# Optimization experiments

Measured on AMD Instinct MI355X. Metric: run time of the kernel, lower is better.

## Reference

```python
import jax, jax.numpy as jnp
import numpy as np

N_NODES = 100000
N_EDGES = 1600000
FEAT = 32
HID = 32
N_GRAPHS = 64


def setup_inputs() -> dict:
    key = jax.random.key(0)
    ks = jax.random.split(key, 12)
    x = jax.random.normal(ks[0], (N_NODES, FEAT), dtype=jnp.float32)
    edge_index = jax.random.randint(ks[1], (2, N_EDGES), 0, N_NODES, dtype=jnp.int64)
    batch = jnp.sort(jax.random.randint(ks[2], (N_NODES,), 0, N_GRAPHS, dtype=jnp.int64))
    # ChebConv (K=3) params: one linear per Chebyshev order + shared bias
    W_cheb = jax.random.normal(ks[3], (3, FEAT, HID), dtype=jnp.float32) * 0.1
    b_cheb = jnp.zeros((HID,), dtype=jnp.float32)
    # MLP head 32 -> 1024 -> 512 -> 4
    W1 = jax.random.normal(ks[4], (HID, 1024), dtype=jnp.float32) * 0.05
    b1 = jnp.zeros((1024,), dtype=jnp.float32)
    W2 = jax.random.normal(ks[5], (1024, 512), dtype=jnp.float32) * 0.05
    b2 = jnp.zeros((512,), dtype=jnp.float32)
    W3 = jax.random.normal(ks[6], (512, 4), dtype=jnp.float32) * 0.05
    b3 = jnp.zeros((4,), dtype=jnp.float32)
    return {"x": x, "edge_index": edge_index, "batch": batch,
            "W_cheb": W_cheb, "b_cheb": b_cheb,
            "W1": W1, "b1": b1, "W2": W2, "b2": b2, "W3": W3, "b3": b3}


def reference(x, edge_index, batch, W_cheb, b_cheb, W1, b1, W2, b2, W3, b3):
    row, col = edge_index[0], edge_index[1]  # source, target
    n = x.shape[0]
    # symmetric normalization of scaled Laplacian (lambda_max=2, no self loops):
    # L_hat = -D^{-1/2} A D^{-1/2}
    deg = jax.ops.segment_sum(jnp.ones((row.shape[0],), x.dtype), row, num_segments=n)
    dis = jnp.where(deg > 0, jax.lax.rsqrt(jnp.where(deg > 0, deg, 1.0)), 0.0)
    norm = -(dis[row] * dis[col])  # [E]

    def prop(h):  # L_hat @ h via gather -> scale -> scatter-add
        return jax.ops.segment_sum(norm[:, None] * h[row], col, num_segments=n)

    # Chebyshev recursion: T0=x, T1=L_hat x, T2=2 L_hat T1 - T0
    Tx0 = x
    Tx1 = prop(Tx0)
    Tx2 = 2.0 * prop(Tx1) - Tx0
    h = Tx0 @ W_cheb[0] + Tx1 @ W_cheb[1] + Tx2 @ W_cheb[2] + b_cheb  # [N, HID]
    # global max pool per graph
    g = jax.ops.segment_max(h, batch, num_segments=N_GRAPHS)  # [B, HID]
    # MLP head (dropout/LeakyReLU defined but unused in original forward)
    h1 = jax.nn.relu(g @ W1 + b1)
    h2 = jax.nn.relu(h1 @ W2 + b2)
    return h2 @ W3 + b3  # [B, 4]
```

## Files before the change

### kernel.cpp

```cpp
#include <hip/hip_runtime.h>
#include <hip/hip_fp16.h>


#define NT 256
#define NTS 1024
#define BSHIFT 8
#define BSIZE 256
#define HB 256
#define CAPC 48
#define CAPR 64
#define CAP 5120

typedef _Float16 half8 __attribute__((ext_vector_type(8)));
typedef float f32x4 __attribute__((ext_vector_type(4)));

__device__ __forceinline__ void atomicMaxFloat(float* addr, float val) {
    if (val >= 0.0f) atomicMax((int*)addr, __float_as_int(val));
    else             atomicMin((unsigned int*)addr, __float_as_uint(val));
}

#define ACC8(raw)                                        \
    do {                                                 \
        const __half2* hp_ = (const __half2*)&(raw);     \
        float2 f0_ = __half22float2(hp_[0]);             \
        float2 f1_ = __half22float2(hp_[1]);             \
        float2 f2_ = __half22float2(hp_[2]);             \
        float2 f3_ = __half22float2(hp_[3]);             \
        a0 += f0_.x; a1 += f0_.y; a2 += f1_.x; a3 += f1_.y; \
        a4 += f2_.x; a5 += f2_.y; a6 += f3_.x; a7 += f3_.y; \
    } while (0)

__global__ __launch_bounds__(512) void k_init(float* __restrict__ g,
                                              const float* __restrict__ Wc,
                                              _Float16* __restrict__ wfrag,
                                              int* __restrict__ bcur,
                                              int* __restrict__ rcur, int NBK) {
    int tid = threadIdx.x;
    for (int i = tid; i < 64 * 32; i += 512) g[i] = -__builtin_inff();
    if (tid < 384) {
        int combo = tid >> 6, lane = tid & 63;
        int mat = combo >> 1, n = combo & 1;
        int m = lane & 15, quad = lane >> 4;
        #pragma unroll
        for (int j = 0; j < 8; j++)
            wfrag[(size_t)combo * 512 + lane * 8 + j] =
                (_Float16)Wc[mat * 1024 + (quad * 8 + j) * 32 + n * 16 + m];
    }
    if (tid < NBK) {
        bcur[tid] = tid * CAP;
        rcur[tid] = tid * CAP;
    }
}

__global__ __launch_bounds__(NTS) void k_bscatter(const int* __restrict__ row,
                                                  const int* __restrict__ col,
                                                  int* __restrict__ bcur,
                                                  int* __restrict__ rcur,
                                                  int* __restrict__ ebuck,
                                                  unsigned char* __restrict__ rbuck,
                                                  int E, int NBK, int epb) {
    __shared__ int cntc[512], cntr[512];
    __shared__ int basec[512], baser[512];
    __shared__ int cstage[512 * CAPC];
    __shared__ unsigned char rstage[512 * CAPR];
    int tid = threadIdx.x;
    if (tid < 512) { cntc[tid] = 0; cntr[tid] = 0; }
    __syncthreads();
    int start = blockIdx.x * epb;
    int end = min(start + epb, E);
    for (int e = start + tid; e < end; e += NTS) {
        int r = row[e], c = col[e];
        int bc_ = c >> BSHIFT;
        int li = atomicAdd(&cntc[bc_], 1);
        if (li < CAPC)
            cstage[bc_ * CAPC + li] = (r << BSHIFT) | (c & (BSIZE - 1));
        int br_ = r >> BSHIFT;
        int lj = atomicAdd(&cntr[br_], 1);
        if (lj < CAPR)
            rstage[br_ * CAPR + lj] = (unsigned char)(r & (BSIZE - 1));
    }
    __syncthreads();
    if (tid < 512) {
        int n = min(cntc[tid], CAPC);
        basec[tid] = n ? atomicAdd(&bcur[tid], n) : 0;
    } else {
        int b = tid - 512;
        int n = min(cntr[b], CAPR);
        baser[b] = n ? atomicAdd(&rcur[b], n) : 0;
    }
    __syncthreads();
    int warp = tid >> 6, lane = tid & 63;
    for (int b = warp; b < NBK; b += (NTS >> 6)) {
        int n = min(cntc[b], CAPC);
        int base = basec[b];
        for (int i = lane; i < n; i += 64)
            ebuck[base + i] = cstage[b * CAPC + i];
    }
    for (int b = warp; b < NBK; b += (NTS >> 6)) {
        int n = min(cntr[b], CAPR);
        int base = baser[b];
        for (int i = lane; i < n; i += 64)
            rbuck[base + i] = rstage[b * CAPR + i];
    }
}

__global__ __launch_bounds__(NT) void k_prep(
    const int* __restrict__ rcur, const unsigned char* __restrict__ rbuck,
    const int* __restrict__ bcur, const int* __restrict__ ebuck,
    const float* __restrict__ x,
    float* __restrict__ dis, float* __restrict__ rdis,
    __half* __restrict__ xh, __half* __restrict__ xsh,
    int* __restrict__ offs, int* __restrict__ entries, int N) {
    __shared__ int cnt[1024];
    __shared__ int tsum[256];
    __shared__ float sdis[256];
    int b = blockIdx.x, tid = threadIdx.x;
    int rbase = b * CAP, rend = rcur[b];
    int ebase = b * CAP, eend = bcur[b];
    cnt[tid] = 0; cnt[tid + 256] = 0; cnt[tid + 512] = 0; cnt[tid + 768] = 0;
    __syncthreads();
    for (int e = rbase + tid; e < rend; e += NT)
        atomicAdd(&cnt[rbuck[e]], 1);
    __syncthreads();
    int dcount = cnt[tid];
    int node = (b << BSHIFT) + tid;
    float d = (dcount > 0) ? rsqrtf((float)dcount) : 0.0f;
    if (node < N) {
        dis[node] = d;
        rdis[node] = (dcount > 0) ? sqrtf((float)dcount) : 0.0f;
    }
    sdis[tid] = d;
    __syncthreads();
    cnt[tid] = 0; cnt[tid + 256] = 0; cnt[tid + 512] = 0; cnt[tid + 768] = 0;
    __syncthreads();
    for (int e = ebase + tid; e < eend; e += NT) {
        int pv = ebuck[e];
        atomicAdd(&cnt[((pv & (BSIZE - 1)) << 2) | ((pv >> BSHIFT) >> 15)], 1);
    }
    __syncthreads();
    int s0 = cnt[tid * 4], s1 = cnt[tid * 4 + 1], s2 = cnt[tid * 4 + 2], s3 = cnt[tid * 4 + 3];
    int tot = s0 + s1 + s2 + s3;
    tsum[tid] = tot;
    __syncthreads();
    for (int off = 1; off < 256; off <<= 1) {
        int t = (tid >= off) ? tsum[tid - off] : 0;
        __syncthreads();
        tsum[tid] += t;
        __syncthreads();
    }
    int excl = tsum[tid] - tot;
    if (node < N) offs[node] = ((ebase + excl) << 9) | tot;
    cnt[tid * 4]     = ebase + excl;
    cnt[tid * 4 + 1] = ebase + excl + s0;
    cnt[tid * 4 + 2] = ebase + excl + s0 + s1;
    cnt[tid * 4 + 3] = ebase + excl + s0 + s1 + s2;
    __syncthreads();
    for (int e = ebase + tid; e < eend; e += NT) {
        int pv = ebuck[e];
        int src = pv >> BSHIFT;
        int li = atomicAdd(&cnt[((pv & (BSIZE - 1)) << 2) | (src >> 15)], 1);
        entries[li] = src;
    }
    int nodebase = b << BSHIFT;
    for (int i4 = tid; i4 < 2048; i4 += NT) {
        int gnode = nodebase + (i4 >> 3);
        if (gnode >= N) break;
        float4 v = ((const float4*)x)[(size_t)nodebase * 8 + i4];
        float dd = sdis[i4 >> 3];
        float2 o, os;
        ((__half2*)&o)[0] = __floats2half2_rn(v.x, v.y);
        ((__half2*)&o)[1] = __floats2half2_rn(v.z, v.w);
        ((__half2*)&os)[0] = __floats2half2_rn(dd * v.x, dd * v.y);
        ((__half2*)&os)[1] = __floats2half2_rn(dd * v.z, dd * v.w);
        ((float2*)xh)[(size_t)nodebase * 8 + i4] = o;
        ((float2*)xsh)[(size_t)nodebase * 8 + i4] = os;
    }
}

__global__ __launch_bounds__(NT) void k_prop1(const int* __restrict__ offs,
                                              const int* __restrict__ entries,
                                              const float* __restrict__ dis,
                                              const __half* __restrict__ xsh,
                                              __half* __restrict__ xs2h, int N) {
    int idx = blockIdx.x * blockDim.x + threadIdx.x;
    int node = idx >> 3, sp = (idx >> 2) & 1, q = idx & 3;
    if (node >= N) return;
    int pv = offs[node];
    int s = pv >> 9, deg = pv & 511;
    int mid = s + (deg >> 1), t = s + deg;
    int lo = sp ? mid : s;
    int hi = sp ? t : mid;
    float a0 = 0, a1 = 0, a2 = 0, a3 = 0, a4 = 0, a5 = 0, a6 = 0, a7 = 0;
    int e = lo;
    for (; e + 4 <= hi; e += 4) {
        int r0 = entries[e], r1 = entries[e + 1], r2 = entries[e + 2], r3 = entries[e + 3];
        float4 w0 = *(const float4*)(xsh + (size_t)r0 * 32 + q * 8);
        float4 w1 = *(const float4*)(xsh + (size_t)r1 * 32 + q * 8);
        float4 w2 = *(const float4*)(xsh + (size_t)r2 * 32 + q * 8);
        float4 w3 = *(const float4*)(xsh + (size_t)r3 * 32 + q * 8);
        ACC8(w0); ACC8(w1); ACC8(w2); ACC8(w3);
    }
    for (; e < hi; e++) {
        int r = entries[e];
        float4 w = *(const float4*)(xsh + (size_t)r * 32 + q * 8);
        ACC8(w);
    }
    a0 += __shfl_xor(a0, 4); a1 += __shfl_xor(a1, 4);
    a2 += __shfl_xor(a2, 4); a3 += __shfl_xor(a3, 4);
    a4 += __shfl_xor(a4, 4); a5 += __shfl_xor(a5, 4);
    a6 += __shfl_xor(a6, 4); a7 += __shfl_xor(a7, 4);
    if (sp == 0) {
        float d = dis[node];
        float sd = -d * d;
        float4 ov;
        ((__half2*)&ov)[0] = __floats2half2_rn(sd * a0, sd * a1);
        ((__half2*)&ov)[1] = __floats2half2_rn(sd * a2, sd * a3);
        ((__half2*)&ov)[2] = __floats2half2_rn(sd * a4, sd * a5);
        ((__half2*)&ov)[3] = __floats2half2_rn(sd * a6, sd * a7);
        *(float4*)(xs2h + (size_t)node * 32 + q * 8) = ov;
    }
}

__global__ __launch_bounds__(NT) void k_combine_f(
    const int* __restrict__ offs, const int* __restrict__ entries,
    const float* __restrict__ dis, const float* __restrict__ rdis,
    const __half* __restrict__ xs2h, const _Float16* __restrict__ xh,
    const _Float16* __restrict__ wfrag, const float* __restrict__ bc,
    const int* __restrict__ batch, float* __restrict__ g, int N) {
    __shared__ float sb[32];
    __shared__ float sp2[64][33];
    __shared__ float hs[64][33];
    __shared__ float lmax[64][32];
    __shared__ int sbatch[64];
    __shared__ int s_blo, s_bhi;

    int tid = threadIdx.x;
    if (tid < 32) sb[tid] = bc[tid];
    int rowbase = blockIdx.x * 64;
    if (tid >= 64 && tid < 128) {
        int gr = rowbase + tid - 64;
        sbatch[tid - 64] = (gr < N) ? batch[gr] : -1;
    }

    int node_l = tid >> 2, q = tid & 3;
    int gnode = rowbase + node_l;
    if (gnode < N) {
        int pv = offs[gnode];
        int s = pv >> 9, t = s + (pv & 511);
        float a0 = 0, a1 = 0, a2 = 0, a3 = 0, a4 = 0, a5 = 0, a6 = 0, a7 = 0;
        int e = s;
        for (; e + 4 <= t; e += 4) {
            int r0 = entries[e], r1 = entries[e + 1], r2 = entries[e + 2], r3 = entries[e + 3];
            float4 w0 = *(const float4*)(xs2h + (size_t)r0 * 32 + q * 8);
            float4 w1 = *(const float4*)(xs2h + (size_t)r1 * 32 + q * 8);
            float4 w2 = *(const float4*)(xs2h + (size_t)r2 * 32 + q * 8);
            float4 w3 = *(const float4*)(xs2h + (size_t)r3 * 32 + q * 8);
            ACC8(w0); ACC8(w1); ACC8(w2); ACC8(w3);
        }
        for (; e < t; e++) {
            int r = entries[e];
            float4 w = *(const float4*)(xs2h + (size_t)r * 32 + q * 8);
            ACC8(w);
        }
        float sc = -dis[gnode];
        float* p = &sp2[node_l][q * 8];
        p[0] = sc * a0; p[1] = sc * a1; p[2] = sc * a2; p[3] = sc * a3;
        p[4] = sc * a4; p[5] = sc * a5; p[6] = sc * a6; p[7] = sc * a7;
    }
    __syncthreads();

    int wave = tid >> 6;
    int lane = tid & 63;
    int m = lane & 15;
    int quad = lane >> 4;
    int grow = rowbase + wave * 16 + m;

    half8 a0 = {}, a1 = {}, a2 = {};
    if (grow < N) {
        size_t off = (size_t)grow * 32 + quad * 8;
        a0 = *(const half8*)(xh + off);
        half8 x2 = *(const half8*)((const _Float16*)xs2h + off);
        float rd = rdis[grow];
        const float* p = &sp2[wave * 16 + m][quad * 8];
        #pragma unroll
        for (int j = 0; j < 8; j++) {
            a1[j] = (_Float16)((float)x2[j] * rd);
            a2[j] = (_Float16)(2.0f * p[j] - (float)a0[j]);
        }
    }

    const half8* wf = (const half8*)wfrag;
    f32x4 acc[2];
    #pragma unroll
    for (int n = 0; n < 2; n++) {
        f32x4 c = {0.f, 0.f, 0.f, 0.f};
        c = __builtin_amdgcn_mfma_f32_16x16x32_f16(a0, wf[(0 * 2 + n) * 64 + lane], c, 0, 0, 0);
        c = __builtin_amdgcn_mfma_f32_16x16x32_f16(a1, wf[(1 * 2 + n) * 64 + lane], c, 0, 0, 0);
        c = __builtin_amdgcn_mfma_f32_16x16x32_f16(a2, wf[(2 * 2 + n) * 64 + lane], c, 0, 0, 0);
        acc[n] = c;
    }

    #pragma unroll
    for (int n = 0; n < 2; n++)
        #pragma unroll
        for (int r = 0; r < 4; r++)
            hs[wave * 16 + quad * 4 + r][n * 16 + m] = acc[n][r] + sb[n * 16 + m];
    if (tid == 0) {
        int lo = sbatch[0];
        int hi = lo;
        for (int j = 63; j > 0; j--) {
            if (sbatch[j] >= 0) { hi = sbatch[j]; break; }
        }
        s_blo = lo; s_bhi = hi;
    }
    __syncthreads();

    int bspan = s_bhi - s_blo + 1;
    for (int i = tid; i < bspan * 32; i += NT) lmax[i >> 5][i & 31] = -__builtin_inff();
    __syncthreads();
    int f = tid & 31, sg = tid >> 5;
    int curb = -1;
    float curm = 0.0f;
    for (int j = sg * 8; j < sg * 8 + 8; j++) {
        int b = sbatch[j];
        if (b < 0) continue;
        float v = hs[j][f];
        if (b != curb) {
            if (curb >= 0) atomicMaxFloat(&lmax[curb - s_blo][f], curm);
            curb = b;
            curm = v;
        } else {
            curm = fmaxf(curm, v);
        }
    }
    if (curb >= 0) atomicMaxFloat(&lmax[curb - s_blo][f], curm);
    __syncthreads();
    for (int i = tid; i < bspan * 32; i += NT) {
        float v = lmax[i >> 5][i & 31];
        if (v > -__builtin_inff()) atomicMaxFloat(&g[(s_blo + (i >> 5)) * 32 + (i & 31)], v);
    }
}

__global__ __launch_bounds__(NT) void k_mlp12(const float* __restrict__ g,
                                              const float* __restrict__ W1,
                                              const float* __restrict__ b1,
                                              const float* __restrict__ W2,
                                              float* __restrict__ h2part) {
    __shared__ float sg[32];
    __shared__ float sh[128];
    int gi = blockIdx.x >> 3, ks = blockIdx.x & 7;
    int tid = threadIdx.x;
    if (tid < 32) sg[tid] = g[gi * 32 + tid];
    __syncthreads();
    if (tid < 128) {
        int c = ks * 128 + tid;
        float a = b1[c];
        #pragma unroll
        for (int k = 0; k < 32; k++) a += sg[k] * W1[k * 1024 + c];
        sh[tid] = fmaxf(a, 0.0f);
    }
    __syncthreads();
    const float* w = W2 + (size_t)(ks * 128) * 512;
    float acc0 = 0.0f, acc1 = 0.0f;
    for (int k = 0; k < 128; k++) {
        float h = sh[k];
        acc0 += h * w[k * 512 + tid];
        acc1 += h * w[k * 512 + tid + 256];
    }
    h2part[gi * 4096 + ks * 512 + tid] = acc0;
    h2part[gi * 4096 + ks * 512 + tid + 256] = acc1;
}

__global__ __launch_bounds__(NT) void k_mlp3p(const float* __restrict__ h2part,
                                              const float* __restrict__ b2,
                                              const float* __restrict__ W3,
                                              const float* __restrict__ b3,
                                              float* __restrict__ out) {
    __shared__ float sh2[512];
    __shared__ float sp[256];
    int gi = blockIdx.x;
    int tid = threadIdx.x;
    for (int k = tid; k < 512; k += NT) {
        float s = 0.0f;
        #pragma unroll
        for (int p = 0; p < 8; p++) s += h2part[gi * 4096 + p * 512 + k];
        sh2[k] = fmaxf(s + b2[k], 0.0f);
    }
    __syncthreads();
    int j = tid & 3, slot = tid >> 2;
    float part = 0.0f;
    #pragma unroll
    for (int kk = 0; kk < 8; kk++) {
        int k = slot * 8 + kk;
        part += sh2[k] * W3[k * 4 + j];
    }
    sp[tid] = part;
    __syncthreads();
    for (int s = 32; s >= 1; s >>= 1) {
        if (slot < s) sp[tid] += sp[(slot + s) * 4 + j];
        __syncthreads();
    }
    if (slot == 0) out[gi * 4 + j] = sp[j] + b3[j];
}

extern "C" void kernel_launch(void* const* d_in, const int* in_sizes, int n_in,
                              void* d_out, int out_size, void* d_ws, size_t ws_size,
                              hipStream_t stream) {
    const float* x   = (const float*)d_in[0];
    const int* ei    = (const int*)d_in[1];
    const int* batch = (const int*)d_in[2];
    const float* Wc  = (const float*)d_in[3];
    const float* bc  = (const float*)d_in[4];
    const float* W1  = (const float*)d_in[5];
    const float* b1  = (const float*)d_in[6];
    const float* W2  = (const float*)d_in[7];
    const float* b2  = (const float*)d_in[8];
    const float* W3  = (const float*)d_in[9];
    const float* b3  = (const float*)d_in[10];
    float* out       = (float*)d_out;

    const int N = in_sizes[2];
    const int E = in_sizes[1] / 2;
    const int* row = ei;
    const int* col = ei + E;
    const int NBK = (N + BSIZE - 1) / BSIZE;
    const int epb = (E + HB - 1) / HB;
    const size_t PADE = (size_t)NBK * CAP;

    float* h2part   = (float*)d_ws;
    int* bcur       = (int*)(h2part + 64 * 4096);
    int* rcur       = bcur + 512;
    float* dis      = (float*)(rcur + 512);
    float* rdis     = dis + N;
    int* offs       = (int*)(rdis + N);
    int* ebuck      = offs + N + 4;
    unsigned char* rbuck = (unsigned char*)(ebuck + PADE);
    int* entries    = (int*)(rbuck + PADE);
    _Float16* xh    = (_Float16*)(entries + PADE);
    _Float16* xsh   = xh + (size_t)N * 32;
    _Float16* xs2h  = xsh + (size_t)N * 32;
    float* g        = (float*)(xs2h + (size_t)N * 32);
    _Float16* wfrag = (_Float16*)(g + 64 * 32);

    k_init<<<1, 512, 0, stream>>>(g, Wc, wfrag, bcur, rcur, NBK);
    k_bscatter<<<HB, NTS, 0, stream>>>(row, col, bcur, rcur, ebuck, rbuck, E, NBK, epb);
    k_prep<<<NBK, NT, 0, stream>>>(rcur, rbuck, bcur, ebuck, x, dis, rdis,
                                   (__half*)xh, (__half*)xsh, offs, entries, N);
    k_prop1<<<((size_t)N * 8 + NT - 1) / NT, NT, 0, stream>>>(offs, entries, dis, (const __half*)xsh, (__half*)xs2h, N);
    k_combine_f<<<(N + 63) / 64, NT, 0, stream>>>(offs, entries, dis, rdis, (const __half*)xs2h, xh, wfrag, bc, batch, g, N);
    k_mlp12<<<512, NT, 0, stream>>>(g, W1, b1, W2, h2part);
    k_mlp3p<<<64, NT, 0, stream>>>(h2part, b2, W3, b3, out);
}
```

Measured before the change: 192.2 us.

## Split edge loops across more threads, wave-shuffle scan, and pair graphs in MLP

```diff
diff --git a/kernel.cpp b/kernel.cpp
--- a/kernel.cpp
+++ b/kernel.cpp
@@ -112,7 +112,7 @@
     __half* __restrict__ xh, __half* __restrict__ xsh,
     int* __restrict__ offs, int* __restrict__ entries, int N) {
     __shared__ int cnt[1024];
-    __shared__ int tsum[256];
+    __shared__ int wsum[4];
     __shared__ float sdis[256];
     int b = blockIdx.x, tid = threadIdx.x;
     int rbase = b * CAP, rend = rcur[b];
@@ -140,15 +140,19 @@
     __syncthreads();
     int s0 = cnt[tid * 4], s1 = cnt[tid * 4 + 1], s2 = cnt[tid * 4 + 2], s3 = cnt[tid * 4 + 3];
     int tot = s0 + s1 + s2 + s3;
-    tsum[tid] = tot;
-    __syncthreads();
-    for (int off = 1; off < 256; off <<= 1) {
-        int t = (tid >= off) ? tsum[tid - off] : 0;
-        __syncthreads();
-        tsum[tid] += t;
-        __syncthreads();
-    }
-    int excl = tsum[tid] - tot;
+    int lane = tid & 63, wv = tid >> 6;
+    int v = tot;
+    #pragma unroll
+    for (int off = 1; off < 64; off <<= 1) {
+        int t = __shfl_up(v, off);
+        if (lane >= off) v += t;
+    }
+    if (lane == 63) wsum[wv] = v;
+    __syncthreads();
+    int wbase = 0;
+    #pragma unroll
+    for (int i = 0; i < 3; i++) wbase += (i < wv) ? wsum[i] : 0;
+    int excl = (v - tot) + wbase;
     if (node < N) offs[node] = ((ebase + excl) << 9) | tot;
     cnt[tid * 4]     = ebase + excl;
     cnt[tid * 4 + 1] = ebase + excl + s0;
@@ -165,13 +169,13 @@
     for (int i4 = tid; i4 < 2048; i4 += NT) {
         int gnode = nodebase + (i4 >> 3);
         if (gnode >= N) break;
-        float4 v = ((const float4*)x)[(size_t)nodebase * 8 + i4];
+        float4 v4 = ((const float4*)x)[(size_t)nodebase * 8 + i4];
         float dd = sdis[i4 >> 3];
         float2 o, os;
-        ((__half2*)&o)[0] = __floats2half2_rn(v.x, v.y);
-        ((__half2*)&o)[1] = __floats2half2_rn(v.z, v.w);
-        ((__half2*)&os)[0] = __floats2half2_rn(dd * v.x, dd * v.y);
-        ((__half2*)&os)[1] = __floats2half2_rn(dd * v.z, dd * v.w);
+        ((__half2*)&o)[0] = __floats2half2_rn(v4.x, v4.y);
+        ((__half2*)&o)[1] = __floats2half2_rn(v4.z, v4.w);
+        ((__half2*)&os)[0] = __floats2half2_rn(dd * v4.x, dd * v4.y);
+        ((__half2*)&os)[1] = __floats2half2_rn(dd * v4.z, dd * v4.w);
         ((float2*)xh)[(size_t)nodebase * 8 + i4] = o;
         ((float2*)xsh)[(size_t)nodebase * 8 + i4] = os;
     }
@@ -183,13 +187,12 @@
                                               const __half* __restrict__ xsh,
                                               __half* __restrict__ xs2h, int N) {
     int idx = blockIdx.x * blockDim.x + threadIdx.x;
-    int node = idx >> 3, sp = (idx >> 2) & 1, q = idx & 3;
+    int node = idx >> 4, spq = (idx >> 2) & 3, q = idx & 3;
     if (node >= N) return;
     int pv = offs[node];
     int s = pv >> 9, deg = pv & 511;
-    int mid = s + (deg >> 1), t = s + deg;
-    int lo = sp ? mid : s;
-    int hi = sp ? t : mid;
+    int lo = s + ((deg * spq) >> 2);
+    int hi = s + ((deg * (spq + 1)) >> 2);
     float a0 = 0, a1 = 0, a2 = 0, a3 = 0, a4 = 0, a5 = 0, a6 = 0, a7 = 0;
     int e = lo;
     for (; e + 4 <= hi; e += 4) {
@@ -209,7 +212,11 @@
     a2 += __shfl_xor(a2, 4); a3 += __shfl_xor(a3, 4);
     a4 += __shfl_xor(a4, 4); a5 += __shfl_xor(a5, 4);
     a6 += __shfl_xor(a6, 4); a7 += __shfl_xor(a7, 4);
-    if (sp == 0) {
+    a0 += __shfl_xor(a0, 8); a1 += __shfl_xor(a1, 8);
+    a2 += __shfl_xor(a2, 8); a3 += __shfl_xor(a3, 8);
+    a4 += __shfl_xor(a4, 8); a5 += __shfl_xor(a5, 8);
+    a6 += __shfl_xor(a6, 8); a7 += __shfl_xor(a7, 8);
+    if (spq == 0) {
         float d = dis[node];
         float sd = -d * d;
         float4 ov;
@@ -228,28 +235,31 @@
     const _Float16* __restrict__ wfrag, const float* __restrict__ bc,
     const int* __restrict__ batch, float* __restrict__ g, int N) {
     __shared__ float sb[32];
-    __shared__ float sp2[64][33];
-    __shared__ float hs[64][33];
+    __shared__ float sp2[32][33];
+    __shared__ float hs[32][33];
     __shared__ float lmax[64][32];
-    __shared__ int sbatch[64];
+    __shared__ int sbatch[32];
     __shared__ int s_blo, s_bhi;
 
     int tid = threadIdx.x;
     if (tid < 32) sb[tid] = bc[tid];
-    int rowbase = blockIdx.x * 64;
-    if (tid >= 64 && tid < 128) {
+    int rowbase = blockIdx.x * 32;
+    if (tid >= 64 && tid < 96) {
         int gr = rowbase + tid - 64;
         sbatch[tid - 64] = (gr < N) ? batch[gr] : -1;
     }
 
-    int node_l = tid >> 2, q = tid & 3;
+    int node_l = tid >> 3, sp = (tid >> 2) & 1, q = tid & 3;
     int gnode = rowbase + node_l;
     if (gnode < N) {
         int pv = offs[gnode];
-        int s = pv >> 9, t = s + (pv & 511);
+        int s = pv >> 9, deg = pv & 511;
+        int mid = s + (deg >> 1), t = s + deg;
+        int lo = sp ? mid : s;
+        int hi = sp ? t : mid;
         float a0 = 0, a1 = 0, a2 = 0, a3 = 0, a4 = 0, a5 = 0, a6 = 0, a7 = 0;
-        int e = s;
-        for (; e + 4 <= t; e += 4) {
+        int e = lo;
+        for (; e + 4 <= hi; e += 4) {
             int r0 = entries[e], r1 = entries[e + 1], r2 = entries[e + 2], r3 = entries[e + 3];
             float4 w0 = *(const float4*)(xs2h + (size_t)r0 * 32 + q * 8);
             float4 w1 = *(const float4*)(xs2h + (size_t)r1 * 32 + q * 8);
@@ -257,15 +267,21 @@
             float4 w3 = *(const float4*)(xs2h + (size_t)r3 * 32 + q * 8);
             ACC8(w0); ACC8(w1); ACC8(w2); ACC8(w3);
         }
-        for (; e < t; e++) {
+        for (; e < hi; e++) {
             int r = entries[e];
             float4 w = *(const float4*)(xs2h + (size_t)r * 32 + q * 8);
             ACC8(w);
         }
-        float sc = -dis[gnode];
-        float* p = &sp2[node_l][q * 8];
-        p[0] = sc * a0; p[1] = sc * a1; p[2] = sc * a2; p[3] = sc * a3;
-        p[4] = sc * a4; p[5] = sc * a5; p[6] = sc * a6; p[7] = sc * a7;
+        a0 += __shfl_xor(a0, 4); a1 += __shfl_xor(a1, 4);
+        a2 += __shfl_xor(a2, 4); a3 += __shfl_xor(a3, 4);
+        a4 += __shfl_xor(a4, 4); a5 += __shfl_xor(a5, 4);
+        a6 += __shfl_xor(a6, 4); a7 += __shfl_xor(a7, 4);
+        if (sp == 0) {
+            float sc = -dis[gnode];
+            float* p = &sp2[node_l][q * 8];
+            p[0] = sc * a0; p[1] = sc * a1; p[2] = sc * a2; p[3] = sc * a3;
+            p[4] = sc * a4; p[5] = sc * a5; p[6] = sc * a6; p[7] = sc * a7;
+        }
     }
     __syncthreads();
 
@@ -273,42 +289,41 @@
     int lane = tid & 63;
     int m = lane & 15;
     int quad = lane >> 4;
-    int grow = rowbase + wave * 16 + m;
-
-    half8 a0 = {}, a1 = {}, a2 = {};
-    if (grow < N) {
-        size_t off = (size_t)grow * 32 + quad * 8;
-        a0 = *(const half8*)(xh + off);
-        half8 x2 = *(const half8*)((const _Float16*)xs2h + off);
-        float rd = rdis[grow];
-        const float* p = &sp2[wave * 16 + m][quad * 8];
+    if (wave < 2) {
+        int grow = rowbase + wave * 16 + m;
+        half8 a0 = {}, a1 = {}, a2 = {};
+        if (grow < N) {
+            size_t off = (size_t)grow * 32 + quad * 8;
+            a0 = *(const half8*)(xh + off);
+            half8 x2 = *(const half8*)((const _Float16*)xs2h + off);
+            float rd = rdis[grow];
+            const float* p = &sp2[wave * 16 + m][quad * 8];
+            #pragma unroll
+            for (int j = 0; j < 8; j++) {
+                a1[j] = (_Float16)((float)x2[j] * rd);
+                a2[j] = (_Float16)(2.0f * p[j] - (float)a0[j]);
+            }
+        }
+        const half8* wf = (const half8*)wfrag;
+        f32x4 acc[2];
         #pragma unroll
-        for (int j = 0; j < 8; j++) {
-            a1[j] = (_Float16)((float)x2[j] * rd);
-            a2[j] = (_Float16)(2.0f * p[j] - (float)a0[j]);
-        }
-    }
-
-    const half8* wf = (const half8*)wfrag;
-    f32x4 acc[2];
-    #pragma unroll
-    for (int n = 0; n < 2; n++) {
-        f32x4 c = {0.f, 0.f, 0.f, 0.f};
-        c = __builtin_amdgcn_mfma_f32_16x16x32_f16(a0, wf[(0 * 2 + n) * 64 + lane], c, 0, 0, 0);
-        c = __builtin_amdgcn_mfma_f32_16x16x32_f16(a1, wf[(1 * 2 + n) * 64 + lane], c, 0, 0, 0);
-        c = __builtin_amdgcn_mfma_f32_16x16x32_f16(a2, wf[(2 * 2 + n) * 64 + lane], c, 0, 0, 0);
-        acc[n] = c;
-    }
-
-    #pragma unroll
-    for (int n = 0; n < 2; n++)
+        for (int n = 0; n < 2; n++) {
+            f32x4 c = {0.f, 0.f, 0.f, 0.f};
+            c = __builtin_amdgcn_mfma_f32_16x16x32_f16(a0, wf[(0 * 2 + n) * 64 + lane], c, 0, 0, 0);
+            c = __builtin_amdgcn_mfma_f32_16x16x32_f16(a1, wf[(1 * 2 + n) * 64 + lane], c, 0, 0, 0);
+            c = __builtin_amdgcn_mfma_f32_16x16x32_f16(a2, wf[(2 * 2 + n) * 64 + lane], c, 0, 0, 0);
+            acc[n] = c;
+        }
         #pragma unroll
-        for (int r = 0; r < 4; r++)
-            hs[wave * 16 + quad * 4 + r][n * 16 + m] = acc[n][r] + sb[n * 16 + m];
+        for (int n = 0; n < 2; n++)
+            #pragma unroll
+            for (int r = 0; r < 4; r++)
+                hs[wave * 16 + quad * 4 + r][n * 16 + m] = acc[n][r] + sb[n * 16 + m];
+    }
     if (tid == 0) {
         int lo = sbatch[0];
         int hi = lo;
-        for (int j = 63; j > 0; j--) {
+        for (int j = 31; j > 0; j--) {
             if (sbatch[j] >= 0) { hi = sbatch[j]; break; }
         }
         s_blo = lo; s_bhi = hi;
@@ -321,7 +336,7 @@
     int f = tid & 31, sg = tid >> 5;
     int curb = -1;
     float curm = 0.0f;
-    for (int j = sg * 8; j < sg * 8 + 8; j++) {
+    for (int j = sg * 4; j < sg * 4 + 4; j++) {
         int b = sbatch[j];
         if (b < 0) continue;
         float v = hs[j][f];
@@ -346,29 +361,40 @@
                                               const float* __restrict__ b1,
                                               const float* __restrict__ W2,
                                               float* __restrict__ h2part) {
-    __shared__ float sg[32];
-    __shared__ float sh[128];
-    int gi = blockIdx.x >> 3, ks = blockIdx.x & 7;
+    __shared__ float sgA[32], sgB[32];
+    __shared__ float shA[128], shB[128];
+    int gp = blockIdx.x >> 3, ks = blockIdx.x & 7;
+    int giA = gp * 2, giB = gp * 2 + 1;
     int tid = threadIdx.x;
-    if (tid < 32) sg[tid] = g[gi * 32 + tid];
+    if (tid < 32) sgA[tid] = g[giA * 32 + tid];
+    else if (tid < 64) sgB[tid - 32] = g[giB * 32 + tid - 32];
     __syncthreads();
     if (tid < 128) {
         int c = ks * 128 + tid;
-        float a = b1[c];
+        float a = b1[c], bacc = b1[c];
         #pragma unroll
-        for (int k = 0; k < 32; k++) a += sg[k] * W1[k * 1024 + c];
-        sh[tid] = fmaxf(a, 0.0f);
+        for (int k = 0; k < 32; k++) {
+            float wv = W1[k * 1024 + c];
+            a += sgA[k] * wv;
+            bacc += sgB[k] * wv;
+        }
+        shA[tid] = fmaxf(a, 0.0f);
+        shB[tid] = fmaxf(bacc, 0.0f);
     }
     __syncthreads();
     const float* w = W2 + (size_t)(ks * 128) * 512;
-    float acc0 = 0.0f, acc1 = 0.0f;
+    float accA0 = 0.0f, accA1 = 0.0f, accB0 = 0.0f, accB1 = 0.0f;
     for (int k = 0; k < 128; k++) {
-        float h = sh[k];
-        acc0 += h * w[k * 512 + tid];
-        acc1 += h * w[k * 512 + tid + 256];
-    }
-    h2part[gi * 4096 + ks * 512 + tid] = acc0;
-    h2part[gi * 4096 + ks * 512 + tid + 256] = acc1;
+        float w0 = w[k * 512 + tid];
+        float w1 = w[k * 512 + tid + 256];
+        float hA = shA[k], hB = shB[k];
+        accA0 += hA * w0; accA1 += hA * w1;
+        accB0 += hB * w0; accB1 += hB * w1;
+    }
+    h2part[giA * 4096 + ks * 512 + tid] = accA0;
+    h2part[giA * 4096 + ks * 512 + tid + 256] = accA1;
+    h2part[giB * 4096 + ks * 512 + tid] = accB0;
+    h2part[giB * 4096 + ks * 512 + tid + 256] = accB1;
 }
 
 __global__ __launch_bounds__(NT) void k_mlp3p(const float* __restrict__ h2part,
@@ -446,8 +472,8 @@
     k_bscatter<<<HB, NTS, 0, stream>>>(row, col, bcur, rcur, ebuck, rbuck, E, NBK, epb);
     k_prep<<<NBK, NT, 0, stream>>>(rcur, rbuck, bcur, ebuck, x, dis, rdis,
                                    (__half*)xh, (__half*)xsh, offs, entries, N);
-    k_prop1<<<((size_t)N * 8 + NT - 1) / NT, NT, 0, stream>>>(offs, entries, dis, (const __half*)xsh, (__half*)xs2h, N);
-    k_combine_f<<<(N + 63) / 64, NT, 0, stream>>>(offs, entries, dis, rdis, (const __half*)xs2h, xh, wfrag, bc, batch, g, N);
-    k_mlp12<<<512, NT, 0, stream>>>(g, W1, b1, W2, h2part);
+    k_prop1<<<((size_t)N * 16 + NT - 1) / NT, NT, 0, stream>>>(offs, entries, dis, (const __half*)xsh, (__half*)xs2h, N);
+    k_combine_f<<<(N + 31) / 32, NT, 0, stream>>>(offs, entries, dis, rdis, (const __half*)xs2h, xh, wfrag, bc, batch, g, N);
+    k_mlp12<<<256, NT, 0, stream>>>(g, W1, b1, W2, h2part);
     k_mlp3p<<<64, NT, 0, stream>>>(h2part, b2, W3, b3, out);
 }
```

New measurement: 192.6 us. Within noise of the previous version (+0.2%).
